# Performance work log

Measured on AMD Instinct MI355X. Metric: run time of the kernel, lower is better.

## Reference

```python
import jax, jax.numpy as jnp
import numpy as np

KAPPA = 5.0
EPS_NORM = 1e-12  # torch F.normalize eps
EPS_LOG = 1e-09


def setup_inputs() -> dict:
    key = jax.random.key(0)
    student_output = jax.random.normal(key, (16384, 256), dtype=jnp.float32)
    return {"student_output": student_output}


def reference(student_output) -> jnp.ndarray:
    # L2-normalize rows (matches F.normalize: x / max(||x||, eps))
    norm = jnp.linalg.norm(student_output, axis=-1, keepdims=True)
    x_norm = student_output / jnp.maximum(norm, EPS_NORM)
    # pairwise cosine similarity [n, n]
    sim = x_norm @ x_norm.T
    kernel = jnp.exp(KAPPA * sim)
    density_estimates = kernel.sum(axis=1)  # [n]
    entropy = -jnp.mean(jnp.log(density_estimates + EPS_LOG))
    return entropy
```

## Files before the change

kernel.cpp:

```cpp
#include <hip/hip_runtime.h>


#define NROWS 16384
#define KDIM 256
#define NTILE 128
#define NT (NROWS / NTILE)
#define NSTRIP 4
#define TOTAL_BLOCKS (NT * NSTRIP)

#define SQRT_KLOG2E 2.68579577857f

typedef int i32x4_t __attribute__((ext_vector_type(4)));
typedef int i32x8_t __attribute__((ext_vector_type(8)));
typedef float f32x16_t __attribute__((ext_vector_type(16)));
typedef __attribute__((address_space(1))) const void global_cvoid_t;
typedef __attribute__((address_space(3))) void lds_void_t;

#if __has_builtin(__builtin_amdgcn_exp2f)
#define EXP2(x) __builtin_amdgcn_exp2f(x)
#else
#define EXP2(x) exp2f(x)
#endif

union frag8 { i32x8_t v8; i32x4_t v4[2]; };

__global__ __launch_bounds__(256)
void kde_normalize(const float* __restrict__ X, unsigned int* __restrict__ Xn8,
                   float* __restrict__ density, unsigned int* __restrict__ ticket) {
  const int wave = threadIdx.x >> 6;
  const int lane = threadIdx.x & 63;
  const int row = blockIdx.x * 4 + wave;
  const float4 v = ((const float4*)(X + (size_t)row * KDIM))[lane];
  float ss = v.x * v.x + v.y * v.y + v.z * v.z + v.w * v.w;
  ss += __shfl_xor(ss, 1);
  ss += __shfl_xor(ss, 2);
  ss += __shfl_xor(ss, 4);
  ss += __shfl_xor(ss, 8);
  ss += __shfl_xor(ss, 16);
  ss += __shfl_xor(ss, 32);
  const float scale = SQRT_KLOG2E / fmaxf(sqrtf(ss), 1e-12f);
  int p = 0;
  p = __builtin_amdgcn_cvt_pk_fp8_f32(v.x * scale, v.y * scale, p, false);
  p = __builtin_amdgcn_cvt_pk_fp8_f32(v.z * scale, v.w * scale, p, true);
  Xn8[(size_t)row * 64 + lane] = (unsigned int)p;
  if (threadIdx.x < 4) density[blockIdx.x * 4 + threadIdx.x] = 0.0f;
  if (blockIdx.x == 0 && threadIdx.x == 0) *ticket = 0u;
}

__global__ __launch_bounds__(256, 2)
void kde_gemm(const unsigned char* __restrict__ Xn8, float* __restrict__ density,
              unsigned int* __restrict__ ticket, float* __restrict__ out) {
  extern __shared__ char smem[];
  char* buf0 = smem;
  char* buf1 = smem + 32768;

  const int tid = threadIdx.x;
  const int wave = tid >> 6;
  const int lane = tid & 63;
  const int wr = wave >> 1;
  const int wc = wave & 1;
  const int m32 = lane & 31;
  const int h = lane >> 5;
  const int bi = blockIdx.x;
  const int s = blockIdx.y;
  const int t0 = s * 16;
  const int nt = (s == NSTRIP - 1 && bi < NT / 2) ? 17 : 16;
  const char* Xb = (const char*)Xn8;

#define STAGE(base_row, dst)                                                      \
  for (int c = wave; c < 32; c += 4) {                                            \
    const int rt = c >> 3, kb = (c >> 1) & 3, hh = c & 1;                         \
    const size_t gofs =                                                           \
        (size_t)((base_row) + rt * 32 + m32) * KDIM + kb * 64 + h * 32 + hh * 16; \
    __builtin_amdgcn_global_load_lds((global_cvoid_t*)(Xb + gofs),                \
                                     (lds_void_t*)((dst) + c * 1024), 16, 0, 0);  \
  }

  STAGE(bi * NTILE, buf0);
  STAGE(((bi + t0) & (NT - 1)) * NTILE, buf1);
  __syncthreads();

  frag8 areg[2][4];
#pragma unroll
  for (int i = 0; i < 2; i++)
#pragma unroll
    for (int kb = 0; kb < 4; kb++) {
      const char* pa = buf0 + ((wr * 2 + i) * 8 + kb * 2) * 1024 + lane * 16;
      areg[i][kb].v4[0] = *(const i32x4_t*)pa;
      areg[i][kb].v4[1] = *(const i32x4_t*)(pa + 1024);
    }
  __syncthreads();

  float rs[2][16];
#pragma unroll
  for (int i = 0; i < 2; i++)
#pragma unroll
    for (int r = 0; r < 16; r++) rs[i][r] = 0.0f;

  for (int k = 0; k < nt; ++k) {
    const int t = t0 + k;
    const int J = (bi + t) & (NT - 1);
    char* rbuf = (k & 1) ? buf0 : buf1;
    char* sbuf = (k & 1) ? buf1 : buf0;

    if (k + 1 < nt) STAGE(((J + 1) & (NT - 1)) * NTILE, sbuf);

    f32x16_t acc[2][2];
#pragma unroll
    for (int i = 0; i < 2; i++)
#pragma unroll
      for (int j = 0; j < 2; j++) acc[i][j] = (f32x16_t)0.0f;

#pragma unroll
    for (int kb = 0; kb < 4; ++kb) {
      frag8 bf[2];
#pragma unroll
      for (int j = 0; j < 2; j++) {
        const char* pb = rbuf + ((wc * 2 + j) * 8 + kb * 2) * 1024 + lane * 16;
        bf[j].v4[0] = *(const i32x4_t*)pb;
        bf[j].v4[1] = *(const i32x4_t*)(pb + 1024);
      }
#pragma unroll
      for (int i = 0; i < 2; i++)
#pragma unroll
        for (int j = 0; j < 2; j++)
          acc[i][j] = __builtin_amdgcn_mfma_scale_f32_32x32x64_f8f6f4(
              areg[i][kb].v8, bf[j].v8, acc[i][j], 0, 0, 0, 127, 0, 127);
    }

    float cs[2] = {0.0f, 0.0f};
#pragma unroll
    for (int i = 0; i < 2; i++)
#pragma unroll
      for (int j = 0; j < 2; j++)
#pragma unroll
        for (int r = 0; r < 16; r++) {
          const float e = EXP2(acc[i][j][r]);
          rs[i][r] += e;
          cs[j] += e;
        }

    if (t != 0) {
#pragma unroll
      for (int j = 0; j < 2; j++) {
        float v = cs[j] + __shfl_xor(cs[j], 32);
        if (h == 0)
          atomicAdd(&density[J * NTILE + wc * 64 + j * 32 + m32], v);
      }
    }

    __syncthreads();
  }

#pragma unroll
  for (int i = 0; i < 2; i++)
#pragma unroll
    for (int r = 0; r < 16; r++) {
      float v = rs[i][r];
      v += __shfl_xor(v, 1);
      v += __shfl_xor(v, 2);
      v += __shfl_xor(v, 4);
      v += __shfl_xor(v, 8);
      v += __shfl_xor(v, 16);
      if (m32 == 0) {
        const int row = bi * NTILE + wr * 64 + i * 32 + (r & 3) + 8 * (r >> 2) + 4 * h;
        atomicAdd(&density[row], v);
      }
    }
#undef STAGE

  __syncthreads();
  if (tid == 0) {
    __threadfence();
    ((volatile unsigned int*)smem)[0] = atomicAdd(ticket, 1u);
  }
  __syncthreads();
  if (((volatile unsigned int*)smem)[0] == TOTAL_BLOCKS - 1) {
    __threadfence();
    float ssum = 0.0f;
    for (int i = tid; i < NROWS; i += 256) {
      const float d = __hip_atomic_load(&density[i], __ATOMIC_RELAXED,
                                        __HIP_MEMORY_SCOPE_AGENT);
      ssum += logf(d + 1e-9f);
    }
    ssum += __shfl_xor(ssum, 1);
    ssum += __shfl_xor(ssum, 2);
    ssum += __shfl_xor(ssum, 4);
    ssum += __shfl_xor(ssum, 8);
    ssum += __shfl_xor(ssum, 16);
    ssum += __shfl_xor(ssum, 32);
    float* red = ((float*)smem) + 16;
    if (lane == 0) red[wave] = ssum;
    __syncthreads();
    if (tid == 0) out[0] = -(red[0] + red[1] + red[2] + red[3]) / (float)NROWS;
  }
}

extern "C" void kernel_launch(void* const* d_in, const int* in_sizes, int n_in,
                              void* d_out, int out_size, void* d_ws, size_t ws_size,
                              hipStream_t stream) {
  const float* X = (const float*)d_in[0];
  float* out = (float*)d_out;
  char* ws = (char*)d_ws;
  unsigned int* Xn8 = (unsigned int*)ws;
  float* density = (float*)(ws + (size_t)NROWS * KDIM);
  unsigned int* ticket = (unsigned int*)(density + NROWS);

  hipFuncSetAttribute((const void*)kde_gemm,
                      hipFuncAttributeMaxDynamicSharedMemorySize, 65536);

  kde_normalize<<<NROWS / 4, 256, 0, stream>>>(X, Xn8, density, ticket);
  kde_gemm<<<dim3(NT, NSTRIP), 256, 65536, stream>>>((const unsigned char*)ws,
                                                     density, ticket, out);
}
```

Before: 133.7 us.

## Split GEMM tile across eight waves with half-height per-wave subtiles

The fused similarity/exp kernel now uses 512 threads per block. Each wave owns a 32x64 subtile instead of 64x64, which halves the A-fragment, accumulator and row-sum registers per wave and adds waves to hide MFMA and exp latency. The leftover 17th tile moves to strip 0, with the tile index remapped to the correct position, and staging and the final reduction are adjusted for 8 waves. The launch bound (512,4) may force a tight VGPR budget that causes spills. Each wave also reuses less data per B-fragment load from LDS.

```diff
diff --git a/kernel.cpp b/kernel.cpp
--- a/kernel.cpp
+++ b/kernel.cpp
@@ -47,7 +47,7 @@
   if (blockIdx.x == 0 && threadIdx.x == 0) *ticket = 0u;
 }
 
-__global__ __launch_bounds__(256, 2)
+__global__ __launch_bounds__(512, 4)
 void kde_gemm(const unsigned char* __restrict__ Xn8, float* __restrict__ density,
               unsigned int* __restrict__ ticket, float* __restrict__ out) {
   extern __shared__ char smem[];
@@ -64,11 +64,11 @@
   const int bi = blockIdx.x;
   const int s = blockIdx.y;
   const int t0 = s * 16;
-  const int nt = (s == NSTRIP - 1 && bi < NT / 2) ? 17 : 16;
+  const int nt = (s == 0 && bi < NT / 2) ? 17 : 16;
   const char* Xb = (const char*)Xn8;
 
 #define STAGE(base_row, dst)                                                      \
-  for (int c = wave; c < 32; c += 4) {                                            \
+  for (int c = wave; c < 32; c += 8) {                                            \
     const int rt = c >> 3, kb = (c >> 1) & 3, hh = c & 1;                         \
     const size_t gofs =                                                           \
         (size_t)((base_row) + rt * 32 + m32) * KDIM + kb * 64 + h * 32 + hh * 16; \
@@ -80,36 +80,33 @@
   STAGE(((bi + t0) & (NT - 1)) * NTILE, buf1);
   __syncthreads();
 
-  frag8 areg[2][4];
-#pragma unroll
-  for (int i = 0; i < 2; i++)
-#pragma unroll
-    for (int kb = 0; kb < 4; kb++) {
-      const char* pa = buf0 + ((wr * 2 + i) * 8 + kb * 2) * 1024 + lane * 16;
-      areg[i][kb].v4[0] = *(const i32x4_t*)pa;
-      areg[i][kb].v4[1] = *(const i32x4_t*)(pa + 1024);
-    }
-  __syncthreads();
-
-  float rs[2][16];
-#pragma unroll
-  for (int i = 0; i < 2; i++)
-#pragma unroll
-    for (int r = 0; r < 16; r++) rs[i][r] = 0.0f;
+  frag8 areg[4];
+#pragma unroll
+  for (int kb = 0; kb < 4; kb++) {
+    const char* pa = buf0 + (wr * 8 + kb * 2) * 1024 + lane * 16;
+    areg[kb].v4[0] = *(const i32x4_t*)pa;
+    areg[kb].v4[1] = *(const i32x4_t*)(pa + 1024);
+  }
+  __syncthreads();
+
+  float rs[16];
+#pragma unroll
+  for (int r = 0; r < 16; r++) rs[r] = 0.0f;
 
   for (int k = 0; k < nt; ++k) {
-    const int t = t0 + k;
+    const int t = t0 + (k == 16 ? 48 : k) + (k == 16 ? 16 : 0);
     const int J = (bi + t) & (NT - 1);
     char* rbuf = (k & 1) ? buf0 : buf1;
     char* sbuf = (k & 1) ? buf1 : buf0;
 
-    if (k + 1 < nt) STAGE(((J + 1) & (NT - 1)) * NTILE, sbuf);
-
-    f32x16_t acc[2][2];
-#pragma unroll
-    for (int i = 0; i < 2; i++)
-#pragma unroll
-      for (int j = 0; j < 2; j++) acc[i][j] = (f32x16_t)0.0f;
+    if (k + 1 < nt) {
+      const int tn = t0 + (k + 1 == 16 ? 64 : k + 1);
+      STAGE(((bi + tn) & (NT - 1)) * NTILE, sbuf);
+    }
+
+    f32x16_t acc[2];
+#pragma unroll
+    for (int j = 0; j < 2; j++) acc[j] = (f32x16_t)0.0f;
 
 #pragma unroll
     for (int kb = 0; kb < 4; ++kb) {
@@ -121,24 +118,20 @@
         bf[j].v4[1] = *(const i32x4_t*)(pb + 1024);
       }
 #pragma unroll
-      for (int i = 0; i < 2; i++)
-#pragma unroll
-        for (int j = 0; j < 2; j++)
-          acc[i][j] = __builtin_amdgcn_mfma_scale_f32_32x32x64_f8f6f4(
-              areg[i][kb].v8, bf[j].v8, acc[i][j], 0, 0, 0, 127, 0, 127);
+      for (int j = 0; j < 2; j++)
+        acc[j] = __builtin_amdgcn_mfma_scale_f32_32x32x64_f8f6f4(
+            areg[kb].v8, bf[j].v8, acc[j], 0, 0, 0, 127, 0, 127);
     }
 
     float cs[2] = {0.0f, 0.0f};
 #pragma unroll
-    for (int i = 0; i < 2; i++)
-#pragma unroll
-      for (int j = 0; j < 2; j++)
-#pragma unroll
-        for (int r = 0; r < 16; r++) {
-          const float e = EXP2(acc[i][j][r]);
-          rs[i][r] += e;
-          cs[j] += e;
-        }
+    for (int j = 0; j < 2; j++)
+#pragma unroll
+      for (int r = 0; r < 16; r++) {
+        const float e = EXP2(acc[j][r]);
+        rs[r] += e;
+        cs[j] += e;
+      }
 
     if (t != 0) {
 #pragma unroll
@@ -153,20 +146,18 @@
   }
 
 #pragma unroll
-  for (int i = 0; i < 2; i++)
-#pragma unroll
-    for (int r = 0; r < 16; r++) {
-      float v = rs[i][r];
-      v += __shfl_xor(v, 1);
-      v += __shfl_xor(v, 2);
-      v += __shfl_xor(v, 4);
-      v += __shfl_xor(v, 8);
-      v += __shfl_xor(v, 16);
-      if (m32 == 0) {
-        const int row = bi * NTILE + wr * 64 + i * 32 + (r & 3) + 8 * (r >> 2) + 4 * h;
-        atomicAdd(&density[row], v);
-      }
-    }
+  for (int r = 0; r < 16; r++) {
+    float v = rs[r];
+    v += __shfl_xor(v, 1);
+    v += __shfl_xor(v, 2);
+    v += __shfl_xor(v, 4);
+    v += __shfl_xor(v, 8);
+    v += __shfl_xor(v, 16);
+    if (m32 == 0) {
+      const int row = bi * NTILE + wr * 32 + (r & 3) + 8 * (r >> 2) + 4 * h;
+      atomicAdd(&density[row], v);
+    }
+  }
 #undef STAGE
 
   __syncthreads();
@@ -178,7 +169,7 @@
   if (((volatile unsigned int*)smem)[0] == TOTAL_BLOCKS - 1) {
     __threadfence();
     float ssum = 0.0f;
-    for (int i = tid; i < NROWS; i += 256) {
+    for (int i = tid; i < NROWS; i += 512) {
       const float d = __hip_atomic_load(&density[i], __ATOMIC_RELAXED,
                                         __HIP_MEMORY_SCOPE_AGENT);
       ssum += logf(d + 1e-9f);
@@ -192,7 +183,11 @@
     float* red = ((float*)smem) + 16;
     if (lane == 0) red[wave] = ssum;
     __syncthreads();
-    if (tid == 0) out[0] = -(red[0] + red[1] + red[2] + red[3]) / (float)NROWS;
+    if (tid == 0) {
+      float tot = 0.0f;
+      for (int w = 0; w < 8; w++) tot += red[w];
+      out[0] = -tot / (float)NROWS;
+    }
   }
 }
 
@@ -210,6 +205,6 @@
                       hipFuncAttributeMaxDynamicSharedMemorySize, 65536);
 
   kde_normalize<<<NROWS / 4, 256, 0, stream>>>(X, Xn8, density, ticket);
-  kde_gemm<<<dim3(NT, NSTRIP), 256, 65536, stream>>>((const unsigned char*)ws,
+  kde_gemm<<<dim3(NT, NSTRIP), 512, 65536, stream>>>((const unsigned char*)ws,
                                                      density, ticket, out);
 }
```

Result: faster. 124.5 us (-6.9%).
